# Optimization experiments

Measured on AMD Instinct MI355X. Metric: run time of the kernel, lower is better.

Reference implementation:

```python
import jax, jax.numpy as jnp
import numpy as np


def setup_inputs() -> dict:
    key = jax.random.key(0)
    kq, kk, kv = jax.random.split(key, 3)
    B, H, S, D = 4, 16, 2048, 64
    q = jax.random.normal(kq, (B, H, S, D), dtype=jnp.float32)
    k = jax.random.normal(kk, (B, H, S, D), dtype=jnp.float32)
    v = jax.random.normal(kv, (B, H, S, D), dtype=jnp.float32)
    # causal mask: True = attend, broadcasts over batch/head dims
    mask = jnp.tril(jnp.ones((S, S), dtype=bool))
    return {"q": q, "k": k, "v": v, "mask": mask}


def reference(q, k, v, mask):
    # att[b,h,i,j] = q[b,h,i,:] . k[b,h,j,:] / sqrt(d_k)
    scale = 1.0 / jnp.sqrt(jnp.asarray(k.shape[-1], dtype=q.dtype))
    att = jnp.einsum('bhqd,bhkd->bhqk', q, k) * scale
    att = jnp.where(mask, att, -jnp.inf)  # additive -inf mask, equivalent to att + where(mask,0,-inf)
    att = jax.nn.softmax(att, axis=-1)
    return jnp.einsum('bhqk,bhkd->bhqd', att, v)
```

## Files before the change

### kernel.cpp

```cpp
#include <hip/hip_runtime.h>
#include <hip/hip_bf16.h>

typedef __attribute__((ext_vector_type(4)))  float f32x4;
typedef __attribute__((ext_vector_type(16))) float f32x16;
typedef __attribute__((ext_vector_type(8)))  short bf16x8;
typedef __attribute__((ext_vector_type(4)))  short bf16x4;

constexpr int SEQ = 2048;
constexpr int DH  = 64;
constexpr int BH  = 64;
constexpr int QB  = 128;
constexpr int KB  = 64;
constexpr int NQT = SEQ / QB;
constexpr int NST = SEQ / 64;

__device__ __forceinline__ short f2bf(float f) {
    union { float f; unsigned u; } x; x.f = f;
    unsigned r = x.u + 0x7fffu + ((x.u >> 16) & 1u);
    return (short)(r >> 16);
}

__device__ __forceinline__ unsigned cvtpk(float lo, float hi) {
    unsigned r;
    asm("v_cvt_pk_bf16_f32 %0, %1, %2" : "=v"(r) : "v"(lo), "v"(hi));
    return r;
}

__device__ __forceinline__ float exp2fast(float x) {
#if __has_builtin(__builtin_amdgcn_exp2f)
    return __builtin_amdgcn_exp2f(x);
#else
    float r;
    asm("v_exp_f32 %0, %1\n\ts_nop 0" : "=v"(r) : "v"(x));
    return r;
#endif
}

__device__ __forceinline__ void half_swap(unsigned a, unsigned b, unsigned &x, unsigned &y) {
#if __has_builtin(__builtin_amdgcn_permlane32_swap)
    auto rr = __builtin_amdgcn_permlane32_swap(a, b, false, false);
    x = rr[0]; y = rr[1];
#else
    unsigned as = (unsigned)__shfl_xor((int)a, 32);
    unsigned bs = (unsigned)__shfl_xor((int)b, 32);
    const bool lo = ((threadIdx.x & 63) < 32);
    x = lo ? a : bs;
    y = lo ? as : b;
#endif
}

__device__ __forceinline__ float sumhalf(float v) {
#if __has_builtin(__builtin_amdgcn_permlane32_swap)
    union { float f; unsigned u; } a; a.f = v;
    auto rr = __builtin_amdgcn_permlane32_swap(a.u, a.u, false, false);
    union { unsigned u; float f; } x, y;
    x.u = rr[0]; y.u = rr[1];
    return x.f + y.f;
#else
    return v + __shfl_xor(v, 32);
#endif
}

__global__ __launch_bounds__(256) void prep_kernel(
    const float* __restrict__ Kg, const float* __restrict__ Vg,
    short* __restrict__ Kb, short* __restrict__ Vt)
{
    __shared__ short sT[64][66];
    const int bid = blockIdx.x;
    const int bh  = bid & (BH - 1);
    const int st  = bid >> 6;
    const int s0  = st * 64;
    const size_t base = (size_t)bh * SEQ * DH;
    const int tid = threadIdx.x;

    #pragma unroll
    for (int it = 0; it < 4; ++it) {
        const int i4 = it * 256 + tid;
        const int r  = i4 >> 4;
        const int c4 = (i4 & 15) << 2;
        const size_t gidx = base + (size_t)(s0 + r) * DH + c4;
        f32x4 kx = *(const f32x4*)(Kg + gidx);
        bf16x4 kb4;
        #pragma unroll
        for (int j = 0; j < 4; ++j) kb4[j] = f2bf(kx[j]);
        *(bf16x4*)(Kb + gidx) = kb4;
        f32x4 vx = *(const f32x4*)(Vg + gidx);
        #pragma unroll
        for (int j = 0; j < 4; ++j) sT[r][c4 + j] = f2bf(vx[j]);
    }
    __syncthreads();

    const int d   = tid >> 2;
    const int seg = (tid & 3) * 16;
    bf16x8 lo, hi;
    #pragma unroll
    for (int m = 0; m < 8; ++m) { lo[m] = sT[seg + m][d]; hi[m] = sT[seg + 8 + m][d]; }
    short* Vo = Vt + base + (size_t)d * SEQ + (s0 + seg);
    *(bf16x8*)Vo       = lo;
    *(bf16x8*)(Vo + 8) = hi;
}

__global__ __launch_bounds__(256, 4) void fattn10_kernel(
    const float* __restrict__ Qg, const short* __restrict__ Kb,
    const short* __restrict__ Vt, float* __restrict__ Og)
{
    __shared__ short sK[2][KB * DH];
    __shared__ short sV[2][DH * KB];

    const int bid  = blockIdx.x;
    const int xcd  = bid & 7;
    const int pass = bid >> 8;
    const int slot = (bid >> 3) & 31;
    const int bh   = xcd * 8 + (slot >> 2);
    const int a    = slot & 3;
    const int qt   = (pass == 0) ? (15 - a) : (pass == 1) ? (8 + a)
                   : (pass == 2) ? (7 - a)  : a;
    const int q0   = qt * QB;

    const int tid  = threadIdx.x;
    const int wid  = tid >> 6;
    const int lane = tid & 63;
    const int l31  = lane & 31;
    const int hi   = lane >> 5;

    const size_t base = (size_t)bh * SEQ * DH;
    const float* Qb = Qg + base;
    const short* Kp = Kb + base;
    const short* Vp = Vt + base;

    const int qw = q0 + wid * 32;
    const int qr = qw + l31;

    const int rrow = wid * 16 + (lane >> 3);
    const int cs   = (lane & 7) ^ (rrow & 7);
    const short* kSrc = Kp + (size_t)rrow * DH + cs * 8;
    const short* vSrc = Vp + (size_t)rrow * SEQ + cs * 8;

    auto ISSUE = [&](int t, int buf) {
        const int kv0 = t * KB;
        __builtin_amdgcn_global_load_lds((const unsigned int*)(kSrc + (size_t)kv0 * DH),
                                         (unsigned int*)&sK[buf][wid * 1024], 16, 0, 0);
        __builtin_amdgcn_global_load_lds((const unsigned int*)(kSrc + (size_t)kv0 * DH + 8 * DH),
                                         (unsigned int*)&sK[buf][wid * 1024 + 512], 16, 0, 0);
        __builtin_amdgcn_global_load_lds((const unsigned int*)(vSrc + kv0),
                                         (unsigned int*)&sV[buf][wid * 1024], 16, 0, 0);
        __builtin_amdgcn_global_load_lds((const unsigned int*)(vSrc + kv0 + 8 * SEQ),
                                         (unsigned int*)&sV[buf][wid * 1024 + 512], 16, 0, 0);
    };

    ISSUE(0, 0);

    constexpr float QSCALE = 0.125f * 1.44269504088896340736f;
    bf16x8 qf[4];
    #pragma unroll
    for (int dt = 0; dt < 4; ++dt) {
        const float* qp = Qb + (size_t)qr * DH + dt * 16 + hi * 8;
        f32x4 av = *(const f32x4*)qp;
        f32x4 bv = *(const f32x4*)(qp + 4);
        bf16x8 f;
        #pragma unroll
        for (int j = 0; j < 4; ++j) { f[j] = f2bf(av[j] * QSCALE); f[j + 4] = f2bf(bv[j] * QSCALE); }
        qf[dt] = f;
    }

    f32x16 z16;
    #pragma unroll
    for (int r = 0; r < 16; ++r) z16[r] = 0.f;

    f32x16 o0, o1;
    #pragma unroll
    for (int r = 0; r < 16; ++r) { o0[r] = 0.f; o1[r] = 0.f; }
    float l_i = 0.f;

    const int ntile = 2 * qt + 2;
    __syncthreads();

    for (int t = 0; t < ntile; ++t) {
        const int kv0 = t * KB;
        const int cur = t & 1;
        if (t + 1 < ntile) ISSUE(t + 1, cur ^ 1);

        if (kv0 <= qw + 31) {
            const short* cK = &sK[cur][0];
            const short* cV = &sV[cur][0];

            f32x16 st0, st1;
            __builtin_amdgcn_s_setprio(1);
            {
                const int ca0 = hi * 16;
                bf16x8 k0 = *(const bf16x8*)((const char*)cK + l31 * 128 + (ca0 ^ ((l31 & 7) << 4)));
                bf16x8 k1 = *(const bf16x8*)((const char*)cK + (32 + l31) * 128 + (ca0 ^ ((l31 & 7) << 4)));
                st0 = __builtin_amdgcn_mfma_f32_32x32x16_bf16(k0, qf[0], z16, 0, 0, 0);
                st1 = __builtin_amdgcn_mfma_f32_32x32x16_bf16(k1, qf[0], z16, 0, 0, 0);
            }
            #pragma unroll
            for (int dt = 1; dt < 4; ++dt) {
                const int ca = dt * 32 + hi * 16;
                bf16x8 k0 = *(const bf16x8*)((const char*)cK + l31 * 128 + (ca ^ ((l31 & 7) << 4)));
                bf16x8 k1 = *(const bf16x8*)((const char*)cK + (32 + l31) * 128 + (ca ^ ((l31 & 7) << 4)));
                st0 = __builtin_amdgcn_mfma_f32_32x32x16_bf16(k0, qf[dt], st0, 0, 0, 0);
                st1 = __builtin_amdgcn_mfma_f32_32x32x16_bf16(k1, qf[dt], st1, 0, 0, 0);
            }
            __builtin_amdgcn_s_setprio(0);

            if (kv0 + KB - 1 > qw) {
                #pragma unroll
                for (int r = 0; r < 16; ++r) {
                    const int kr = (r & 3) + 8 * (r >> 2) + 4 * hi;
                    if (kv0 + kr > qr)      st0[r] = -1e30f;
                    if (kv0 + 32 + kr > qr) st1[r] = -1e30f;
                }
            }

            float rs0 = 0.f, rs1 = 0.f, rs2 = 0.f, rs3 = 0.f;
            #pragma unroll
            for (int r = 0; r < 16; r += 4) {
                st0[r]     = exp2fast(st0[r]);     rs0 += st0[r];
                st0[r + 1] = exp2fast(st0[r + 1]); rs1 += st0[r + 1];
                st0[r + 2] = exp2fast(st0[r + 2]); rs2 += st0[r + 2];
                st0[r + 3] = exp2fast(st0[r + 3]); rs3 += st0[r + 3];
            }
            #pragma unroll
            for (int r = 0; r < 16; r += 4) {
                st1[r]     = exp2fast(st1[r]);     rs0 += st1[r];
                st1[r + 1] = exp2fast(st1[r + 1]); rs1 += st1[r + 1];
                st1[r + 2] = exp2fast(st1[r + 2]); rs2 += st1[r + 2];
                st1[r + 3] = exp2fast(st1[r + 3]); rs3 += st1[r + 3];
            }
            l_i += sumhalf((rs0 + rs1) + (rs2 + rs3));

            bf16x8 pf[4];
            {
                unsigned pk[8];
                #pragma unroll
                for (int i = 0; i < 8; ++i) pk[i] = cvtpk(st0[2 * i], st0[2 * i + 1]);
                #pragma unroll
                for (int cc = 0; cc < 2; ++cc) {
                    unsigned x0, y0, x1, y1;
                    half_swap(pk[4 * cc + 0], pk[4 * cc + 2], x0, y0);
                    half_swap(pk[4 * cc + 1], pk[4 * cc + 3], x1, y1);
                    union { unsigned u[4]; bf16x8 v; } uu;
                    uu.u[0] = x0; uu.u[1] = x1; uu.u[2] = y0; uu.u[3] = y1;
                    pf[cc] = uu.v;
                }
                #pragma unroll
                for (int i = 0; i < 8; ++i) pk[i] = cvtpk(st1[2 * i], st1[2 * i + 1]);
                #pragma unroll
                for (int cc = 0; cc < 2; ++cc) {
                    unsigned x0, y0, x1, y1;
                    half_swap(pk[4 * cc + 0], pk[4 * cc + 2], x0, y0);
                    half_swap(pk[4 * cc + 1], pk[4 * cc + 3], x1, y1);
                    union { unsigned u[4]; bf16x8 v; } uu;
                    uu.u[0] = x0; uu.u[1] = x1; uu.u[2] = y0; uu.u[3] = y1;
                    pf[2 + cc] = uu.v;
                }
            }

            __builtin_amdgcn_s_setprio(1);
            #pragma unroll
            for (int ks = 0; ks < 4; ++ks) {
                const int cv = ks * 32 + hi * 16;
                bf16x8 v0 = *(const bf16x8*)((const char*)cV + l31 * 128 + (cv ^ ((l31 & 7) << 4)));
                o0 = __builtin_amdgcn_mfma_f32_32x32x16_bf16(pf[ks], v0, o0, 0, 0, 0);
                bf16x8 v1 = *(const bf16x8*)((const char*)cV + (32 + l31) * 128 + (cv ^ ((l31 & 7) << 4)));
                o1 = __builtin_amdgcn_mfma_f32_32x32x16_bf16(pf[ks], v1, o1, 0, 0, 0);
            }
            __builtin_amdgcn_s_setprio(0);
        }

        __syncthreads();
    }

    float* Ob = Og + base;
    #pragma unroll
    for (int r = 0; r < 16; ++r) {
        const int kr  = (r & 3) + 8 * (r >> 2) + 4 * hi;
        const float ll = __shfl(l_i, kr);
        const float inv = 1.0f / ll;
        const int row = qw + kr;
        Ob[(size_t)row * DH + l31]      = o0[r] * inv;
        Ob[(size_t)row * DH + 32 + l31] = o1[r] * inv;
    }
}

extern "C" void kernel_launch(void* const* d_in, const int* in_sizes, int n_in,
                              void* d_out, int out_size, void* d_ws, size_t ws_size,
                              hipStream_t stream) {
    const float* q = (const float*)d_in[0];
    const float* k = (const float*)d_in[1];
    const float* v = (const float*)d_in[2];
    float* out = (float*)d_out;

    short* Kb = (short*)d_ws;
    short* Vt = Kb + (size_t)BH * SEQ * DH;

    prep_kernel<<<dim3(BH * NST), dim3(256), 0, stream>>>(k, v, Kb, Vt);
    fattn10_kernel<<<dim3(BH * NQT), dim3(256), 0, stream>>>(q, Kb, Vt, out);
}
```

Baseline: 71.16 us.

## Use single-wave blocks reading pre-swizzled K/V fragments directly from global memory

The prep kernel now writes K and V in a fragment-ordered tiled layout, so each MFMA operand is one contiguous 16-byte load. The attention kernel becomes one 64-thread wave per 32 query rows, loading K/V straight from global/L2 with no LDS staging, double buffering or barriers. Heaviest query tiles are scheduled first. This removes LDS traffic and barrier stalls but gives up K/V reuse across waves and the async prefetch, so it relies on L2 bandwidth and latency hiding from many resident waves.

```diff
diff --git a/kernel.cpp b/kernel.cpp
--- a/kernel.cpp
+++ b/kernel.cpp
@@ -9,9 +9,6 @@
 constexpr int SEQ = 2048;
 constexpr int DH  = 64;
 constexpr int BH  = 64;
-constexpr int QB  = 128;
-constexpr int KB  = 64;
-constexpr int NQT = SEQ / QB;
 constexpr int NST = SEQ / 64;
 
 __device__ __forceinline__ short f2bf(float f) {
@@ -63,14 +60,15 @@
 
 __global__ __launch_bounds__(256) void prep_kernel(
     const float* __restrict__ Kg, const float* __restrict__ Vg,
-    short* __restrict__ Kb, short* __restrict__ Vt)
+    short* __restrict__ KF, short* __restrict__ VF)
 {
     __shared__ short sT[64][66];
     const int bid = blockIdx.x;
     const int bh  = bid & (BH - 1);
     const int st  = bid >> 6;
     const int s0  = st * 64;
-    const size_t base = (size_t)bh * SEQ * DH;
+    const size_t base  = (size_t)bh * SEQ * DH;
+    const size_t tbase = base + (size_t)st * 4096;
     const int tid = threadIdx.x;
 
     #pragma unroll
@@ -82,73 +80,48 @@
         f32x4 kx = *(const f32x4*)(Kg + gidx);
         bf16x4 kb4;
         #pragma unroll
-        for (int j = 0; j < 4; ++j) kb4[j] = f2bf(kx[j]);
-        *(bf16x4*)(Kb + gidx) = kb4;
+        for (int jj = 0; jj < 4; ++jj) kb4[jj] = f2bf(kx[jj]);
+        *(bf16x4*)(KF + tbase + ((c4 >> 3) << 9) + (r << 3) + (c4 & 7)) = kb4;
         f32x4 vx = *(const f32x4*)(Vg + gidx);
         #pragma unroll
-        for (int j = 0; j < 4; ++j) sT[r][c4 + j] = f2bf(vx[j]);
+        for (int jj = 0; jj < 4; ++jj) sT[r][c4 + jj] = f2bf(vx[jj]);
     }
     __syncthreads();
 
-    const int d   = tid >> 2;
-    const int seg = (tid & 3) * 16;
-    bf16x8 lo, hi;
-    #pragma unroll
-    for (int m = 0; m < 8; ++m) { lo[m] = sT[seg + m][d]; hi[m] = sT[seg + 8 + m][d]; }
-    short* Vo = Vt + base + (size_t)d * SEQ + (s0 + seg);
-    *(bf16x8*)Vo       = lo;
-    *(bf16x8*)(Vo + 8) = hi;
-}
-
-__global__ __launch_bounds__(256, 4) void fattn10_kernel(
-    const float* __restrict__ Qg, const short* __restrict__ Kb,
-    const short* __restrict__ Vt, float* __restrict__ Og)
+    #pragma unroll
+    for (int it = 0; it < 2; ++it) {
+        const int u   = it * 256 + tid;
+        const int sub = u >> 6;
+        const int d   = u & 63;
+        bf16x8 w;
+        #pragma unroll
+        for (int jj = 0; jj < 8; ++jj) w[jj] = sT[sub * 8 + jj][d];
+        *(bf16x8*)(VF + tbase + (sub << 9) + (d << 3)) = w;
+    }
+}
+
+__global__ __launch_bounds__(64, 4) void fattn11_kernel(
+    const float* __restrict__ Qg, const short* __restrict__ KF,
+    const short* __restrict__ VF, float* __restrict__ Og)
 {
-    __shared__ short sK[2][KB * DH];
-    __shared__ short sV[2][DH * KB];
-
-    const int bid  = blockIdx.x;
-    const int xcd  = bid & 7;
-    const int pass = bid >> 8;
-    const int slot = (bid >> 3) & 31;
-    const int bh   = xcd * 8 + (slot >> 2);
-    const int a    = slot & 3;
-    const int qt   = (pass == 0) ? (15 - a) : (pass == 1) ? (8 + a)
-                   : (pass == 2) ? (7 - a)  : a;
-    const int q0   = qt * QB;
-
-    const int tid  = threadIdx.x;
-    const int wid  = tid >> 6;
-    const int lane = tid & 63;
+    const int bid = blockIdx.x;
+    const int xcd = bid & 7;
+    const int j   = bid >> 3;
+    const int bh  = xcd * 8 + (j & 7);
+    const int qwi = 63 - (j >> 3);
+    const int qw  = qwi << 5;
+
+    const int lane = threadIdx.x & 63;
     const int l31  = lane & 31;
     const int hi   = lane >> 5;
 
     const size_t base = (size_t)bh * SEQ * DH;
     const float* Qb = Qg + base;
-    const short* Kp = Kb + base;
-    const short* Vp = Vt + base;
-
-    const int qw = q0 + wid * 32;
-    const int qr = qw + l31;
-
-    const int rrow = wid * 16 + (lane >> 3);
-    const int cs   = (lane & 7) ^ (rrow & 7);
-    const short* kSrc = Kp + (size_t)rrow * DH + cs * 8;
-    const short* vSrc = Vp + (size_t)rrow * SEQ + cs * 8;
-
-    auto ISSUE = [&](int t, int buf) {
-        const int kv0 = t * KB;
-        __builtin_amdgcn_global_load_lds((const unsigned int*)(kSrc + (size_t)kv0 * DH),
-                                         (unsigned int*)&sK[buf][wid * 1024], 16, 0, 0);
-        __builtin_amdgcn_global_load_lds((const unsigned int*)(kSrc + (size_t)kv0 * DH + 8 * DH),
-                                         (unsigned int*)&sK[buf][wid * 1024 + 512], 16, 0, 0);
-        __builtin_amdgcn_global_load_lds((const unsigned int*)(vSrc + kv0),
-                                         (unsigned int*)&sV[buf][wid * 1024], 16, 0, 0);
-        __builtin_amdgcn_global_load_lds((const unsigned int*)(vSrc + kv0 + 8 * SEQ),
-                                         (unsigned int*)&sV[buf][wid * 1024 + 512], 16, 0, 0);
-    };
-
-    ISSUE(0, 0);
+    const short* KFp = KF + base;
+    const short* VFp = VF + base;
+
+    const int qr    = qw + l31;
+    const int ntile = (qwi >> 1) + 1;
 
     constexpr float QSCALE = 0.125f * 1.44269504088896340736f;
     bf16x8 qf[4];
@@ -159,7 +132,7 @@
         f32x4 bv = *(const f32x4*)(qp + 4);
         bf16x8 f;
         #pragma unroll
-        for (int j = 0; j < 4; ++j) { f[j] = f2bf(av[j] * QSCALE); f[j + 4] = f2bf(bv[j] * QSCALE); }
+        for (int jj = 0; jj < 4; ++jj) { f[jj] = f2bf(av[jj] * QSCALE); f[jj + 4] = f2bf(bv[jj] * QSCALE); }
         qf[dt] = f;
     }
 
@@ -172,103 +145,93 @@
     for (int r = 0; r < 16; ++r) { o0[r] = 0.f; o1[r] = 0.f; }
     float l_i = 0.f;
 
-    const int ntile = 2 * qt + 2;
-    __syncthreads();
-
     for (int t = 0; t < ntile; ++t) {
-        const int kv0 = t * KB;
-        const int cur = t & 1;
-        if (t + 1 < ntile) ISSUE(t + 1, cur ^ 1);
-
-        if (kv0 <= qw + 31) {
-            const short* cK = &sK[cur][0];
-            const short* cV = &sV[cur][0];
-
-            f32x16 st0, st1;
-            __builtin_amdgcn_s_setprio(1);
-            {
-                const int ca0 = hi * 16;
-                bf16x8 k0 = *(const bf16x8*)((const char*)cK + l31 * 128 + (ca0 ^ ((l31 & 7) << 4)));
-                bf16x8 k1 = *(const bf16x8*)((const char*)cK + (32 + l31) * 128 + (ca0 ^ ((l31 & 7) << 4)));
-                st0 = __builtin_amdgcn_mfma_f32_32x32x16_bf16(k0, qf[0], z16, 0, 0, 0);
-                st1 = __builtin_amdgcn_mfma_f32_32x32x16_bf16(k1, qf[0], z16, 0, 0, 0);
+        const short* kb = KFp + t * 4096;
+        const short* vb = VFp + t * 4096;
+
+        f32x16 st0, st1;
+        __builtin_amdgcn_s_setprio(1);
+        {
+            const int sub0 = hi;
+            bf16x8 k0 = *(const bf16x8*)(kb + (sub0 << 9) + (l31 << 3));
+            bf16x8 k1 = *(const bf16x8*)(kb + (sub0 << 9) + ((32 + l31) << 3));
+            st0 = __builtin_amdgcn_mfma_f32_32x32x16_bf16(k0, qf[0], z16, 0, 0, 0);
+            st1 = __builtin_amdgcn_mfma_f32_32x32x16_bf16(k1, qf[0], z16, 0, 0, 0);
+        }
+        #pragma unroll
+        for (int dt = 1; dt < 4; ++dt) {
+            const int sub = dt * 2 + hi;
+            bf16x8 k0 = *(const bf16x8*)(kb + (sub << 9) + (l31 << 3));
+            bf16x8 k1 = *(const bf16x8*)(kb + (sub << 9) + ((32 + l31) << 3));
+            st0 = __builtin_amdgcn_mfma_f32_32x32x16_bf16(k0, qf[dt], st0, 0, 0, 0);
+            st1 = __builtin_amdgcn_mfma_f32_32x32x16_bf16(k1, qf[dt], st1, 0, 0, 0);
+        }
+        __builtin_amdgcn_s_setprio(0);
+
+        if (t == ntile - 1) {
+            const int kv0 = t * 64;
+            #pragma unroll
+            for (int r = 0; r < 16; ++r) {
+                const int kr = (r & 3) + 8 * (r >> 2) + 4 * hi;
+                if (kv0 + kr > qr)      st0[r] = -1e30f;
+                if (kv0 + 32 + kr > qr) st1[r] = -1e30f;
             }
-            #pragma unroll
-            for (int dt = 1; dt < 4; ++dt) {
-                const int ca = dt * 32 + hi * 16;
-                bf16x8 k0 = *(const bf16x8*)((const char*)cK + l31 * 128 + (ca ^ ((l31 & 7) << 4)));
-                bf16x8 k1 = *(const bf16x8*)((const char*)cK + (32 + l31) * 128 + (ca ^ ((l31 & 7) << 4)));
-                st0 = __builtin_amdgcn_mfma_f32_32x32x16_bf16(k0, qf[dt], st0, 0, 0, 0);
-                st1 = __builtin_amdgcn_mfma_f32_32x32x16_bf16(k1, qf[dt], st1, 0, 0, 0);
+        }
+
+        float rs0 = 0.f, rs1 = 0.f, rs2 = 0.f, rs3 = 0.f;
+        #pragma unroll
+        for (int r = 0; r < 16; r += 4) {
+            st0[r]     = exp2fast(st0[r]);     rs0 += st0[r];
+            st0[r + 1] = exp2fast(st0[r + 1]); rs1 += st0[r + 1];
+            st0[r + 2] = exp2fast(st0[r + 2]); rs2 += st0[r + 2];
+            st0[r + 3] = exp2fast(st0[r + 3]); rs3 += st0[r + 3];
+        }
+        #pragma unroll
+        for (int r = 0; r < 16; r += 4) {
+            st1[r]     = exp2fast(st1[r]);     rs0 += st1[r];
+            st1[r + 1] = exp2fast(st1[r + 1]); rs1 += st1[r + 1];
+            st1[r + 2] = exp2fast(st1[r + 2]); rs2 += st1[r + 2];
+            st1[r + 3] = exp2fast(st1[r + 3]); rs3 += st1[r + 3];
+        }
+        l_i += sumhalf((rs0 + rs1) + (rs2 + rs3));
+
+        bf16x8 pf[4];
+        {
+            unsigned pk[8];
+            #pragma unroll
+            for (int i = 0; i < 8; ++i) pk[i] = cvtpk(st0[2 * i], st0[2 * i + 1]);
+            #pragma unroll
+            for (int cc = 0; cc < 2; ++cc) {
+                unsigned x0, y0, x1, y1;
+                half_swap(pk[4 * cc + 0], pk[4 * cc + 2], x0, y0);
+                half_swap(pk[4 * cc + 1], pk[4 * cc + 3], x1, y1);
+                union { unsigned u[4]; bf16x8 v; } uu;
+                uu.u[0] = x0; uu.u[1] = x1; uu.u[2] = y0; uu.u[3] = y1;
+                pf[cc] = uu.v;
             }
-            __builtin_amdgcn_s_setprio(0);
-
-            if (kv0 + KB - 1 > qw) {
-                #pragma unroll
-                for (int r = 0; r < 16; ++r) {
-                    const int kr = (r & 3) + 8 * (r >> 2) + 4 * hi;
-                    if (kv0 + kr > qr)      st0[r] = -1e30f;
-                    if (kv0 + 32 + kr > qr) st1[r] = -1e30f;
-                }
+            #pragma unroll
+            for (int i = 0; i < 8; ++i) pk[i] = cvtpk(st1[2 * i], st1[2 * i + 1]);
+            #pragma unroll
+            for (int cc = 0; cc < 2; ++cc) {
+                unsigned x0, y0, x1, y1;
+                half_swap(pk[4 * cc + 0], pk[4 * cc + 2], x0, y0);
+                half_swap(pk[4 * cc + 1], pk[4 * cc + 3], x1, y1);
+                union { unsigned u[4]; bf16x8 v; } uu;
+                uu.u[0] = x0; uu.u[1] = x1; uu.u[2] = y0; uu.u[3] = y1;
+                pf[2 + cc] = uu.v;
             }
-
-            float rs0 = 0.f, rs1 = 0.f, rs2 = 0.f, rs3 = 0.f;
-            #pragma unroll
-            for (int r = 0; r < 16; r += 4) {
-                st0[r]     = exp2fast(st0[r]);     rs0 += st0[r];
-                st0[r + 1] = exp2fast(st0[r + 1]); rs1 += st0[r + 1];
-                st0[r + 2] = exp2fast(st0[r + 2]); rs2 += st0[r + 2];
-                st0[r + 3] = exp2fast(st0[r + 3]); rs3 += st0[r + 3];
-            }
-            #pragma unroll
-            for (int r = 0; r < 16; r += 4) {
-                st1[r]     = exp2fast(st1[r]);     rs0 += st1[r];
-                st1[r + 1] = exp2fast(st1[r + 1]); rs1 += st1[r + 1];
-                st1[r + 2] = exp2fast(st1[r + 2]); rs2 += st1[r + 2];
-                st1[r + 3] = exp2fast(st1[r + 3]); rs3 += st1[r + 3];
-            }
-            l_i += sumhalf((rs0 + rs1) + (rs2 + rs3));
-
-            bf16x8 pf[4];
-            {
-                unsigned pk[8];
-                #pragma unroll
-                for (int i = 0; i < 8; ++i) pk[i] = cvtpk(st0[2 * i], st0[2 * i + 1]);
-                #pragma unroll
-                for (int cc = 0; cc < 2; ++cc) {
-                    unsigned x0, y0, x1, y1;
-                    half_swap(pk[4 * cc + 0], pk[4 * cc + 2], x0, y0);
-                    half_swap(pk[4 * cc + 1], pk[4 * cc + 3], x1, y1);
-                    union { unsigned u[4]; bf16x8 v; } uu;
-                    uu.u[0] = x0; uu.u[1] = x1; uu.u[2] = y0; uu.u[3] = y1;
-                    pf[cc] = uu.v;
-                }
-                #pragma unroll
-                for (int i = 0; i < 8; ++i) pk[i] = cvtpk(st1[2 * i], st1[2 * i + 1]);
-                #pragma unroll
-                for (int cc = 0; cc < 2; ++cc) {
-                    unsigned x0, y0, x1, y1;
-                    half_swap(pk[4 * cc + 0], pk[4 * cc + 2], x0, y0);
-                    half_swap(pk[4 * cc + 1], pk[4 * cc + 3], x1, y1);
-                    union { unsigned u[4]; bf16x8 v; } uu;
-                    uu.u[0] = x0; uu.u[1] = x1; uu.u[2] = y0; uu.u[3] = y1;
-                    pf[2 + cc] = uu.v;
-                }
-            }
-
-            __builtin_amdgcn_s_setprio(1);
-            #pragma unroll
-            for (int ks = 0; ks < 4; ++ks) {
-                const int cv = ks * 32 + hi * 16;
-                bf16x8 v0 = *(const bf16x8*)((const char*)cV + l31 * 128 + (cv ^ ((l31 & 7) << 4)));
-                o0 = __builtin_amdgcn_mfma_f32_32x32x16_bf16(pf[ks], v0, o0, 0, 0, 0);
-                bf16x8 v1 = *(const bf16x8*)((const char*)cV + (32 + l31) * 128 + (cv ^ ((l31 & 7) << 4)));
-                o1 = __builtin_amdgcn_mfma_f32_32x32x16_bf16(pf[ks], v1, o1, 0, 0, 0);
-            }
-            __builtin_amdgcn_s_setprio(0);
-        }
-
-        __syncthreads();
+        }
+
+        __builtin_amdgcn_s_setprio(1);
+        #pragma unroll
+        for (int ks = 0; ks < 4; ++ks) {
+            const int sub = ks * 2 + hi;
+            bf16x8 v0 = *(const bf16x8*)(vb + (sub << 9) + (l31 << 3));
+            o0 = __builtin_amdgcn_mfma_f32_32x32x16_bf16(pf[ks], v0, o0, 0, 0, 0);
+            bf16x8 v1 = *(const bf16x8*)(vb + (sub << 9) + ((32 + l31) << 3));
+            o1 = __builtin_amdgcn_mfma_f32_32x32x16_bf16(pf[ks], v1, o1, 0, 0, 0);
+        }
+        __builtin_amdgcn_s_setprio(0);
     }
 
     float* Ob = Og + base;
@@ -291,9 +254,9 @@
     const float* v = (const float*)d_in[2];
     float* out = (float*)d_out;
 
-    short* Kb = (short*)d_ws;
-    short* Vt = Kb + (size_t)BH * SEQ * DH;
-
-    prep_kernel<<<dim3(BH * NST), dim3(256), 0, stream>>>(k, v, Kb, Vt);
-    fattn10_kernel<<<dim3(BH * NQT), dim3(256), 0, stream>>>(q, Kb, Vt, out);
-}
+    short* KF = (short*)d_ws;
+    short* VF = KF + (size_t)BH * SEQ * DH;
+
+    prep_kernel<<<dim3(BH * NST), dim3(256), 0, stream>>>(k, v, KF, VF);
+    fattn11_kernel<<<dim3(BH * SEQ / 32), dim3(64), 0, stream>>>(q, KF, VF, out);
+}
```

New measurement: 92.63 us. 1.3x slower.
